# Kernel tuning notes

Measured on AMD Instinct MI355X. Metric: run time of the kernel, lower is better.

The kernel has to match this reference:

```python
import jax, jax.numpy as jnp
import numpy as np

# T time steps, N nodes, R relations, E edges per (t, relation)
T, N, IN_DIM, HID, R, E = 6, 50000, 256, 256, 4, 800000


def setup_inputs() -> dict:
    key = jax.random.key(0)
    ks = jax.random.split(key, 12)
    s = 0.05  # weight scale to keep activations well-conditioned
    return {
        "feat": jax.random.normal(ks[0], (T, N, IN_DIM), jnp.float32),
        "edge_row": jax.random.randint(ks[1], (T, R, E), 0, N, jnp.int32),
        "edge_col": jax.random.randint(ks[2], (T, R, E), 0, N, jnp.int32),
        "edge_w": jax.random.uniform(ks[3], (T, R, E), jnp.float32) * 0.1,
        "W_rel": jax.random.normal(ks[4], (R, IN_DIM, HID), jnp.float32) * s,
        "b_rel": jnp.zeros((R, HID), jnp.float32),
        "rel_query": jax.random.normal(ks[5], (HID,), jnp.float32),
        "gru_W_ih": jax.random.normal(ks[6], (3 * HID, HID), jnp.float32) * s,
        "gru_W_hh": jax.random.normal(ks[7], (3 * HID, HID), jnp.float32) * s,
        "gru_b_ih": jnp.zeros((3 * HID,), jnp.float32),
        "gru_b_hh": jnp.zeros((3 * HID,), jnp.float32),
        "W1": jax.random.normal(ks[8], (HID, HID), jnp.float32) * s,
        "b1": jnp.zeros((HID,), jnp.float32),
        "W2": jax.random.normal(ks[9], (HID, 1), jnp.float32) * s,
        "b2": jnp.zeros((1,), jnp.float32),
    }


def reference(feat, edge_row, edge_col, edge_w, W_rel, b_rel, rel_query,
              gru_W_ih, gru_W_hh, gru_b_ih, gru_b_hh, W1, b1, W2, b2):
    n_nodes = feat.shape[1]
    hid = rel_query.shape[0]

    def spatial(x, row, col, w):
        # per-relation dense transform: [R, N, H]
        z = jnp.einsum('ni,rio->rno', x, W_rel) + b_rel[:, None, :]

        # sparse.mm(A_r, z_r): m[i] = sum_e w_e * z[col_e] scattered to row_e
        def agg(z_r, row_r, col_r, w_r):
            return jax.ops.segment_sum(w_r[:, None] * z_r[col_r], row_r,
                                       num_segments=n_nodes)

        msgs = jax.vmap(agg)(z, row, col, w)  # [R, N, H]
        # relation attention: softmax over relation axis
        alpha = jax.nn.softmax(jnp.einsum('rnh,h->rn', msgs, rel_query), axis=0)
        return jax.nn.relu(jnp.einsum('rn,rnh->nh', alpha, msgs))  # [N, H]

    def gru_step(h, x):
        # torch GRU gate order: r, z, n
        gi = x @ gru_W_ih.T + gru_b_ih  # [N, 3H]
        gh = h @ gru_W_hh.T + gru_b_hh
        ir, iz, inn = jnp.split(gi, 3, axis=-1)
        hr, hz, hn = jnp.split(gh, 3, axis=-1)
        r = jax.nn.sigmoid(ir + hr)
        zg = jax.nn.sigmoid(iz + hz)
        ng = jnp.tanh(inn + r * hn)
        return (1.0 - zg) * ng + zg * h

    def step(h, xs):
        x_t, row_t, col_t, w_t = xs
        return gru_step(h, spatial(x_t, row_t, col_t, w_t)), None

    h0 = jnp.zeros((n_nodes, hid), feat.dtype)
    h_last, _ = jax.lax.scan(step, h0, (feat, edge_row, edge_col, edge_w))

    # classifier (dropout is identity in eval mode)
    h1 = jax.nn.relu(h_last @ W1 + b1)
    return (h1 @ W2 + b2)[:, 0]  # [N]
```

## Files before the change

### kernel.cpp

```cpp
#include <hip/hip_runtime.h>
#include <hip/hip_bf16.h>
#include <math.h>

#define T_STEPS 6
#define N_NODES 50000
#define IN_DIM  256
#define HID     256
#define R_REL   4
#define E_EDGES 800000
#define G3      768
#define MPAD    50048
#define NTR     24
#define ETOT    19200000
#define NTOT    1200000
#define NCB_R   98
#define NCB_TOT 2352
#define CH_BLOCKS 2400
#define CH_EDGES  8000
#define CH_PER_TR 100
#define BCAP    10240

typedef unsigned short ushort_t;
typedef _Float16 f16x8 __attribute__((ext_vector_type(8)));
typedef float  f32x4  __attribute__((ext_vector_type(4)));

__device__ __forceinline__ ushort_t f2h(float v) {
    _Float16 h = (_Float16)v;
    ushort_t u;
    __builtin_memcpy(&u, &h, 2);
    return u;
}
__device__ __forceinline__ float h2f(ushort_t u) {
    _Float16 h;
    __builtin_memcpy(&h, &u, 2);
    return (float)h;
}

__global__ void prep_bt(const float* __restrict__ src, ushort_t* __restrict__ hi,
                        ushort_t* __restrict__ lo, int K, int Nc, int transposed) {
    int idx = blockIdx.x * blockDim.x + threadIdx.x;
    if (idx >= K * Nc) return;
    int n = idx / K, k = idx % K;
    float v = transposed ? src[(size_t)n * K + k] : src[(size_t)k * Nc + n];
    ushort_t hh = f2h(v);
    ushort_t ll = f2h(v - h2f(hh));
    hi[idx] = hh;
    lo[idx] = ll;
}

__global__ void pack_feat_h(const float* __restrict__ f, ushort_t* __restrict__ ph,
                            int total4) {
    int idx = blockIdx.x * blockDim.x + threadIdx.x;
    if (idx >= total4) return;
    float4 v = ((const float4*)f)[idx];
    ushort4 o;
    o.x = f2h(v.x); o.y = f2h(v.y); o.z = f2h(v.z); o.w = f2h(v.w);
    ((ushort4*)ph)[idx] = o;
}


__global__ __launch_bounds__(256)
void coarse_fill(const int* __restrict__ row, const int* __restrict__ col,
                 const float* __restrict__ w, int* __restrict__ gcur,
                 int2* __restrict__ brec) {
    __shared__ int cnt[NCB_R], ofs[NCB_R];
    int tr = blockIdx.x / CH_PER_TR;
    int base = blockIdx.x * CH_EDGES;
    for (int i = threadIdx.x; i < NCB_R; i += 256) cnt[i] = 0;
    __syncthreads();
    for (int k = threadIdx.x; k < CH_EDGES; k += 256)
        atomicAdd(&cnt[row[base + k] >> 9], 1);
    __syncthreads();
    if (threadIdx.x < NCB_R) {
        int c = cnt[threadIdx.x];
        int bk = tr * NCB_R + threadIdx.x;
        int g = c ? atomicAdd(&gcur[bk], c) : 0;
        ofs[threadIdx.x] = bk * BCAP + g;
        cnt[threadIdx.x] = 0;
    }
    __syncthreads();
    for (int k = threadIdx.x; k < CH_EDGES; k += 256) {
        int rr = row[base + k];
        int kb = rr >> 9;
        int pos = ofs[kb] + atomicAdd(&cnt[kb], 1);
        brec[pos] = make_int2(col[base + k] | ((rr & 511) << 16),
                              __float_as_int(w[base + k]));
    }
}

__global__ __launch_bounds__(256)
void place_rows(const int2* __restrict__ brec, const int* __restrict__ gcur,
                int2* __restrict__ starts2, unsigned* __restrict__ colw) {
    __shared__ int cnt[512], rofs[512];
    __shared__ unsigned buf[BCAP];
    int b = blockIdx.x;
    int tr = b / NCB_R, rb = b % NCB_R;
    int row0 = rb << 9;
    int nrows = min(512, N_NODES - row0);
    int s0 = b * BCAP;
    int nrec = min(gcur[b], BCAP);
    for (int i = threadIdx.x; i < 512; i += 256) cnt[i] = 0;
    __syncthreads();
    for (int e = threadIdx.x; e < nrec; e += 256)
        atomicAdd(&cnt[(brec[s0 + e].x >> 16) & 511], 1);
    __syncthreads();
    if (threadIdx.x == 0) {
        int run = 0;
        for (int i = 0; i < 512; ++i) { rofs[i] = run; run += cnt[i]; }
    }
    __syncthreads();
    for (int i = threadIdx.x; i < nrows; i += 256)
        starts2[tr * N_NODES + row0 + i] =
            make_int2(s0 + rofs[i], s0 + rofs[i] + cnt[i]);
    __syncthreads();
    for (int i = threadIdx.x; i < 512; i += 256) cnt[i] = 0;
    __syncthreads();
    for (int e = threadIdx.x; e < nrec; e += 256) {
        int2 rec = brec[s0 + e];
        int rl = (rec.x >> 16) & 511;
        int pos = rofs[rl] + atomicAdd(&cnt[rl], 1);
        buf[pos] = (unsigned)(rec.x & 0xFFFF) |
                   ((unsigned)f2h(__int_as_float(rec.y)) << 16);
    }
    __syncthreads();
    for (int i = threadIdx.x; i < nrec; i += 256)
        colw[s0 + i] = buf[i];
}

__global__ void csr_agg_t(const ushort_t* __restrict__ xh, const unsigned* __restrict__ colw,
                          const int2* __restrict__ startsT,
                          ushort_t* __restrict__ tmp, float* __restrict__ rowsum) {
    int wid  = (blockIdx.x * blockDim.x + threadIdx.x) >> 6;
    int lane = threadIdx.x & 63;
    int r    = blockIdx.y;
    if (wid >= N_NODES) return;
    int2 se = startsT[r * N_NODES + wid];
    int s0 = se.x, s1 = se.y;
    float4 acc = make_float4(0.f, 0.f, 0.f, 0.f);
    float wsum = 0.f;
    const ushort_t* xb = xh + (lane << 2);
    int e = s0;
    for (; e + 8 <= s1; e += 8) {
        unsigned rr[8];
#pragma unroll
        for (int k = 0; k < 8; ++k) rr[k] = colw[e + k];
        ushort4 xv[8];
#pragma unroll
        for (int k = 0; k < 8; ++k)
            xv[k] = *(const ushort4*)(xb + ((size_t)(rr[k] & 0xFFFF) << 8));
#pragma unroll
        for (int k = 0; k < 8; ++k) {
            float wk = h2f((ushort_t)(rr[k] >> 16));
            acc.x = fmaf(wk, h2f(xv[k].x), acc.x);
            acc.y = fmaf(wk, h2f(xv[k].y), acc.y);
            acc.z = fmaf(wk, h2f(xv[k].z), acc.z);
            acc.w = fmaf(wk, h2f(xv[k].w), acc.w);
            wsum += wk;
        }
    }
    for (; e + 4 <= s1; e += 4) {
        unsigned rr[4];
#pragma unroll
        for (int k = 0; k < 4; ++k) rr[k] = colw[e + k];
        ushort4 xv[4];
#pragma unroll
        for (int k = 0; k < 4; ++k)
            xv[k] = *(const ushort4*)(xb + ((size_t)(rr[k] & 0xFFFF) << 8));
#pragma unroll
        for (int k = 0; k < 4; ++k) {
            float wk = h2f((ushort_t)(rr[k] >> 16));
            acc.x = fmaf(wk, h2f(xv[k].x), acc.x);
            acc.y = fmaf(wk, h2f(xv[k].y), acc.y);
            acc.z = fmaf(wk, h2f(xv[k].z), acc.z);
            acc.w = fmaf(wk, h2f(xv[k].w), acc.w);
            wsum += wk;
        }
    }
    for (; e < s1; ++e) {
        unsigned rec = colw[e];
        float we = h2f((ushort_t)(rec >> 16));
        ushort4 xv = *(const ushort4*)(xb + ((size_t)(rec & 0xFFFF) << 8));
        acc.x = fmaf(we, h2f(xv.x), acc.x);
        acc.y = fmaf(we, h2f(xv.y), acc.y);
        acc.z = fmaf(we, h2f(xv.z), acc.z);
        acc.w = fmaf(we, h2f(xv.w), acc.w);
        wsum += we;
    }
    ushort4 hv;
    hv.x = f2h(acc.x); hv.y = f2h(acc.y); hv.z = f2h(acc.z); hv.w = f2h(acc.w);
    *(ushort4*)(tmp + ((size_t)r * MPAD + wid) * 256 + lane * 4) = hv;
    if (lane == 0) rowsum[r * MPAD + wid] = wsum;
}

__global__ __launch_bounds__(256, 3)
void mfma_gemm(const ushort_t* __restrict__ Af, const ushort_t* __restrict__ Bthi,
               const ushort_t* __restrict__ Btlo, void* __restrict__ Cv,
               int M, int Nc, const float* __restrict__ bias,
               const float* __restrict__ rowscale, int do_relu, int out16,
               size_t aZ, size_t bZ, size_t cZ, int biasZ, int rsZ) {
    int z = blockIdx.z;
    Af   += (size_t)z * aZ;
    Bthi += (size_t)z * bZ;  Btlo += (size_t)z * bZ;
    if (bias)     bias     += (size_t)z * biasZ;
    if (rowscale) rowscale += (size_t)z * rsZ;

    __shared__ __align__(16) char smem[49152];
    const int AOF = 0, BHI = 16384, BLO = 32768;
    int tid = threadIdx.x;
    int m0 = blockIdx.x * 128, n0 = blockIdx.y * 128;
    int lane = tid & 63, wid = tid >> 6;
    int wr = wid >> 1, wc = wid & 1;
    int lr = lane & 15, lk = lane >> 4;
    int xorv = (lr & 7) << 4;

    f32x4 acc[4][4];
#pragma unroll
    for (int i = 0; i < 4; ++i)
#pragma unroll
        for (int j = 0; j < 4; ++j)
            acc[i][j] = (f32x4){0.f, 0.f, 0.f, 0.f};

    for (int kt = 0; kt < 4; ++kt) {
        int k0 = kt * 64;
        __syncthreads();
#pragma unroll
        for (int i = 0; i < 4; ++i) {
            int c = tid + i * 256;
            int row = c >> 3, slot = c & 7;
            int ldsoff = row * 128 + ((slot * 16) ^ ((row & 7) << 4));
            size_t ga = (size_t)(m0 + row) * 256 + k0 + slot * 8;
            size_t gb = (size_t)(n0 + row) * 256 + k0 + slot * 8;
            *(int4*)(smem + AOF + ldsoff) = *(const int4*)(Af + ga);
            *(int4*)(smem + BHI + ldsoff) = *(const int4*)(Bthi + gb);
            *(int4*)(smem + BLO + ldsoff) = *(const int4*)(Btlo + gb);
        }
        __syncthreads();
#pragma unroll
        for (int kk2 = 0; kk2 < 2; ++kk2) {
            int kb = (kk2 * 64 + lk * 16) ^ xorv;
            f16x8 a[4], bh[4], bl[4];
#pragma unroll
            for (int f = 0; f < 4; ++f) {
                int ra = (wr * 64 + f * 16 + lr) * 128 + kb;
                int rb = (wc * 64 + f * 16 + lr) * 128 + kb;
                a[f]  = *(const f16x8*)(smem + AOF + ra);
                bh[f] = *(const f16x8*)(smem + BHI + rb);
                bl[f] = *(const f16x8*)(smem + BLO + rb);
            }
#pragma unroll
            for (int fm = 0; fm < 4; ++fm)
#pragma unroll
                for (int fn = 0; fn < 4; ++fn) {
                    acc[fm][fn] = __builtin_amdgcn_mfma_f32_16x16x32_f16(a[fm], bh[fn], acc[fm][fn], 0, 0, 0);
                    acc[fm][fn] = __builtin_amdgcn_mfma_f32_16x16x32_f16(a[fm], bl[fn], acc[fm][fn], 0, 0, 0);
                }
        }
    }
    float*    C32 = (float*)Cv    + (size_t)blockIdx.z * cZ;
    ushort_t* C16 = (ushort_t*)Cv + (size_t)blockIdx.z * cZ;
#pragma unroll
    for (int fm = 0; fm < 4; ++fm) {
        int grb = m0 + wr * 64 + fm * 16 + lk * 4;
#pragma unroll
        for (int j = 0; j < 4; ++j) {
            int gr = grb + j;
            if (gr >= M) continue;
            float rs = rowscale ? rowscale[gr] : 1.0f;
#pragma unroll
            for (int fn = 0; fn < 4; ++fn) {
                int gc = n0 + wc * 64 + fn * 16 + lr;
                float v = acc[fm][fn][j];
                if (bias) v += rs * bias[gc];
                if (do_relu) v = fmaxf(v, 0.f);
                if (out16) C16[(size_t)gr * Nc + gc] = f2h(v);
                else       C32[(size_t)gr * Nc + gc] = v;
            }
        }
    }
}

__global__ void attn_combine(const ushort_t* __restrict__ msgs,
                             const float* __restrict__ q,
                             ushort_t* __restrict__ s_f, int N) {
    int n = blockIdx.x, j = threadIdx.x;
    size_t NH = (size_t)N * 256;
    size_t base = (size_t)n * 256 + j;
    float m0 = h2f(msgs[0 * NH + base]);
    float m1 = h2f(msgs[1 * NH + base]);
    float m2 = h2f(msgs[2 * NH + base]);
    float m3 = h2f(msgs[3 * NH + base]);
    float qv = q[j];
    float v0 = m0 * qv, v1 = m1 * qv, v2 = m2 * qv, v3 = m3 * qv;
#pragma unroll
    for (int off = 32; off; off >>= 1) {
        v0 += __shfl_xor(v0, off);
        v1 += __shfl_xor(v1, off);
        v2 += __shfl_xor(v2, off);
        v3 += __shfl_xor(v3, off);
    }
    __shared__ float part[4][4];
    __shared__ float alpha[4];
    int wid = j >> 6, lane = j & 63;
    if (lane == 0) {
        part[0][wid] = v0; part[1][wid] = v1; part[2][wid] = v2; part[3][wid] = v3;
    }
    __syncthreads();
    if (j == 0) {
        float d[4];
#pragma unroll
        for (int r = 0; r < 4; ++r) d[r] = part[r][0] + part[r][1] + part[r][2] + part[r][3];
        float mx = fmaxf(fmaxf(d[0], d[1]), fmaxf(d[2], d[3]));
        float e[4], sum = 0.f;
#pragma unroll
        for (int r = 0; r < 4; ++r) { e[r] = expf(d[r] - mx); sum += e[r]; }
#pragma unroll
        for (int r = 0; r < 4; ++r) alpha[r] = e[r] / sum;
    }
    __syncthreads();
    float sv = alpha[0] * m0 + alpha[1] * m1 + alpha[2] * m2 + alpha[3] * m3;
    s_f[base] = f2h(fmaxf(sv, 0.f));
}

__global__ void gru_gate(const ushort_t* __restrict__ gi, const ushort_t* __restrict__ gh,
                         float* __restrict__ h, ushort_t* __restrict__ h_f,
                         int total4) {
    int idx = blockIdx.x * blockDim.x + threadIdx.x;
    if (idx >= total4) return;
    int i = idx >> 6, j = (idx & 63) * 4;
    size_t b = (size_t)i * 768 + j;
    ushort4 ir4 = *(const ushort4*)(gi + b);
    ushort4 iz4 = *(const ushort4*)(gi + b + 256);
    ushort4 in4 = *(const ushort4*)(gi + b + 512);
    ushort4 hr4 = *(const ushort4*)(gh + b);
    ushort4 hz4 = *(const ushort4*)(gh + b + 256);
    ushort4 hn4 = *(const ushort4*)(gh + b + 512);
    size_t o = (size_t)i * 256 + j;
    float4 hv = *(const float4*)(h + o);
    float4 hnew;
    const ushort_t* irp = &ir4.x; const ushort_t* izp = &iz4.x; const ushort_t* inp = &in4.x;
    const ushort_t* hrp = &hr4.x; const ushort_t* hzp = &hz4.x; const ushort_t* hnp = &hn4.x;
    const float* hvp = &hv.x; float* hop = &hnew.x;
    ushort4 hf4;
    ushort_t* hfp = &hf4.x;
#pragma unroll
    for (int k = 0; k < 4; ++k) {
        float r = 1.f / (1.f + expf(-(h2f(irp[k]) + h2f(hrp[k]))));
        float z = 1.f / (1.f + expf(-(h2f(izp[k]) + h2f(hzp[k]))));
        float ng = tanhf(h2f(inp[k]) + r * h2f(hnp[k]));
        float v = (1.f - z) * ng + z * hvp[k];
        hop[k] = v;
        hfp[k] = f2h(v);
    }
    *(float4*)(h + o) = hnew;
    *(ushort4*)(h_f + o) = hf4;
}

__global__ void classifier_out(const float* __restrict__ h1, const float* __restrict__ W2,
                               const float* __restrict__ b2, float* __restrict__ out, int N) {
    int n = blockIdx.x, j = threadIdx.x;
    float v = h1[(size_t)n * 256 + j] * W2[j];
#pragma unroll
    for (int off = 32; off; off >>= 1) v += __shfl_xor(v, off);
    __shared__ float part[4];
    if ((j & 63) == 0) part[j >> 6] = v;
    __syncthreads();
    if (j == 0) out[n] = part[0] + part[1] + part[2] + part[3] + b2[0];
}

extern "C" void kernel_launch(void* const* d_in, const int* in_sizes, int n_in,
                              void* d_out, int out_size, void* d_ws, size_t ws_size,
                              hipStream_t stream) {
    const float* feat  = (const float*)d_in[0];
    const int*   erow  = (const int*)d_in[1];
    const int*   ecol  = (const int*)d_in[2];
    const float* ew    = (const float*)d_in[3];
    const float* W_rel = (const float*)d_in[4];
    const float* b_rel = (const float*)d_in[5];
    const float* rq    = (const float*)d_in[6];
    const float* Wih   = (const float*)d_in[7];
    const float* Whh   = (const float*)d_in[8];
    const float* bih   = (const float*)d_in[9];
    const float* bhh   = (const float*)d_in[10];
    const float* W1    = (const float*)d_in[11];
    const float* b1    = (const float*)d_in[12];
    const float* W2    = (const float*)d_in[13];
    const float* b2    = (const float*)d_in[14];
    float* out = (float*)d_out;

    const int N = N_NODES;
    char* ws = (char*)d_ws;

    size_t off_msgs   = 0;
    size_t off_gh     = 102400000;
    size_t off_colw   = 179200000;
    size_t off_h      = 275537920;
    size_t off_hf     = 326737920;
    size_t off_sf     = 352362496;
    size_t off_tmp    = 377987072;
    size_t off_rowsum = 480485376;
    size_t off_wrelh  = 481286144;
    size_t off_wrell  = 481810432;
    size_t off_wihh   = 482334720;
    size_t off_wihl   = 482727936;
    size_t off_whhh   = 483121152;
    size_t off_whhl   = 483514368;
    size_t off_w1h    = 483907584;
    size_t off_w1l    = 484038656;
    size_t off_gcur   = 484169728;
    size_t off_starts = 484179152;
    size_t off_feath  = 493779152;
    size_t off_brec   = 647379168;

    ushort_t* msgs   = (ushort_t*)(ws + off_msgs);
    ushort_t* gi     = (ushort_t*)(ws + off_msgs);
    float*    h1     = (float*)(ws + off_msgs);
    ushort_t* gh     = (ushort_t*)(ws + off_gh);
    unsigned* colw   = (unsigned*)(ws + off_colw);
    float*    h      = (float*)(ws + off_h);
    ushort_t* h_f    = (ushort_t*)(ws + off_hf);
    ushort_t* s_f    = (ushort_t*)(ws + off_sf);
    ushort_t* tmp    = (ushort_t*)(ws + off_tmp);
    float*    rowsum = (float*)(ws + off_rowsum);
    ushort_t* wrel_h = (ushort_t*)(ws + off_wrelh);
    ushort_t* wrel_l = (ushort_t*)(ws + off_wrell);
    ushort_t* wih_h  = (ushort_t*)(ws + off_wihh);
    ushort_t* wih_l  = (ushort_t*)(ws + off_wihl);
    ushort_t* whh_h  = (ushort_t*)(ws + off_whhh);
    ushort_t* whh_l  = (ushort_t*)(ws + off_whhl);
    ushort_t* w1_h   = (ushort_t*)(ws + off_w1h);
    ushort_t* w1_l   = (ushort_t*)(ws + off_w1l);
    int*      gcur   = (int*)(ws + off_gcur);
    int2*     starts2= (int2*)(ws + off_starts);
    ushort_t* feath  = (ushort_t*)(ws + off_feath);
    int2*     brec   = (int2*)(ws + off_brec);

    for (int r = 0; r < R_REL; ++r)
        prep_bt<<<(65536 + 255) / 256, 256, 0, stream>>>(
            W_rel + (size_t)r * 65536, wrel_h + (size_t)r * 65536,
            wrel_l + (size_t)r * 65536, 256, 256, 0);
    prep_bt<<<(G3 * 256 + 255) / 256, 256, 0, stream>>>(Wih, wih_h, wih_l, 256, G3, 1);
    prep_bt<<<(G3 * 256 + 255) / 256, 256, 0, stream>>>(Whh, whh_h, whh_l, 256, G3, 1);
    prep_bt<<<(65536 + 255) / 256, 256, 0, stream>>>(W1, w1_h, w1_l, 256, 256, 0);
    pack_feat_h<<<(T_STEPS * N * IN_DIM / 4 + 255) / 256, 256, 0, stream>>>(
        feat, feath, T_STEPS * N * IN_DIM / 4);

    hipMemsetAsync(h, 0, (size_t)N * HID * 4, stream);
    hipMemsetAsync(ws + off_hf, 0, 25624576, stream);
    hipMemsetAsync(gcur, 0, NCB_TOT * 4, stream);

    coarse_fill<<<CH_BLOCKS, 256, 0, stream>>>(erow, ecol, ew, gcur, brec);
    place_rows<<<NCB_TOT, 256, 0, stream>>>(brec, gcur, starts2, colw);

    dim3 g_rel(MPAD / 128, 2, 4);
    dim3 g_g3(MPAD / 128, 6, 1);
    dim3 g_cls(MPAD / 128, 2, 1);
    dim3 agg_grid((N + 3) / 4, 4);

    for (int t = 0; t < T_STEPS; ++t) {
        const ushort_t* xh_t = feath + (size_t)t * N * IN_DIM;
        csr_agg_t<<<agg_grid, 256, 0, stream>>>(
            xh_t, colw, starts2 + (size_t)t * R_REL * N, tmp, rowsum);
        mfma_gemm<<<g_rel, 256, 0, stream>>>(
            tmp, wrel_h, wrel_l, msgs, N, 256, b_rel, rowsum, 0, 1,
            (size_t)MPAD * 256, 65536, (size_t)N * 256, 256, MPAD);
        attn_combine<<<N, 256, 0, stream>>>(msgs, rq, s_f, N);
        mfma_gemm<<<g_g3, 256, 0, stream>>>(s_f, wih_h, wih_l, gi, N, G3,
                                            bih, nullptr, 0, 1, 0, 0, 0, 0, 0);
        mfma_gemm<<<g_g3, 256, 0, stream>>>(h_f, whh_h, whh_l, gh, N, G3,
                                            bhh, nullptr, 0, 1, 0, 0, 0, 0, 0);
        gru_gate<<<(N * 64 + 255) / 256, 256, 0, stream>>>(gi, gh, h, h_f, N * 64);
    }

    mfma_gemm<<<g_cls, 256, 0, stream>>>(h_f, w1_h, w1_l, h1, N, 256,
                                         b1, nullptr, 1, 0, 0, 0, 0, 0, 0);
    classifier_out<<<N, 256, 0, stream>>>(h1, W2, b2, out, N);
}
```

Baseline: 4.454 ms.

## Pre-pack GEMM weights in MFMA fragment order and load B directly from global

Weight matrices are now repacked into MFMA lane-fragment order (hi/lo fp16 split) so each lane can load its B operand as one 16-byte vector straight from global memory. The GEMM no longer stages B hi/lo through LDS, which cuts shared memory from 48KB to 16KB and removes two thirds of the tile-load traffic into LDS. The cost is that B fragments are re-read from global/L2 per wave on every k step instead of being shared through LDS, and the loads now sit in the inner loop rather than being overlapped with the LDS fill.

```diff
diff --git a/kernel.cpp b/kernel.cpp
--- a/kernel.cpp
+++ b/kernel.cpp
@@ -36,16 +36,17 @@
     return (float)h;
 }
 
-__global__ void prep_bt(const float* __restrict__ src, ushort_t* __restrict__ hi,
-                        ushort_t* __restrict__ lo, int K, int Nc, int transposed) {
-    int idx = blockIdx.x * blockDim.x + threadIdx.x;
-    if (idx >= K * Nc) return;
-    int n = idx / K, k = idx % K;
-    float v = transposed ? src[(size_t)n * K + k] : src[(size_t)k * Nc + n];
+__global__ void prep_bt_pack(const float* __restrict__ src, ushort_t* __restrict__ hi,
+                             ushort_t* __restrict__ lo, int Nc, int transposed) {
+    int p = blockIdx.x * blockDim.x + threadIdx.x;
+    if (p >= Nc * 256) return;
+    int j = p & 7, lane = (p >> 3) & 63, k32 = (p >> 9) & 7, nc16 = p >> 12;
+    int col = nc16 * 16 + (lane & 15);
+    int k   = k32 * 32 + (lane >> 4) * 8 + j;
+    float v = transposed ? src[(size_t)col * 256 + k] : src[(size_t)k * Nc + col];
     ushort_t hh = f2h(v);
-    ushort_t ll = f2h(v - h2f(hh));
-    hi[idx] = hh;
-    lo[idx] = ll;
+    hi[p] = hh;
+    lo[p] = f2h(v - h2f(hh));
 }
 
 __global__ void pack_feat_h(const float* __restrict__ f, ushort_t* __restrict__ ph,
@@ -193,25 +194,25 @@
 }
 
 __global__ __launch_bounds__(256, 3)
-void mfma_gemm(const ushort_t* __restrict__ Af, const ushort_t* __restrict__ Bthi,
-               const ushort_t* __restrict__ Btlo, void* __restrict__ Cv,
+void mfma_gemm(const ushort_t* __restrict__ Af, const ushort_t* __restrict__ Bphi,
+               const ushort_t* __restrict__ Bplo, void* __restrict__ Cv,
                int M, int Nc, const float* __restrict__ bias,
                const float* __restrict__ rowscale, int do_relu, int out16,
                size_t aZ, size_t bZ, size_t cZ, int biasZ, int rsZ) {
     int z = blockIdx.z;
     Af   += (size_t)z * aZ;
-    Bthi += (size_t)z * bZ;  Btlo += (size_t)z * bZ;
+    Bphi += (size_t)z * bZ;  Bplo += (size_t)z * bZ;
     if (bias)     bias     += (size_t)z * biasZ;
     if (rowscale) rowscale += (size_t)z * rsZ;
 
-    __shared__ __align__(16) char smem[49152];
-    const int AOF = 0, BHI = 16384, BLO = 32768;
+    __shared__ __align__(16) char smem[16384];
     int tid = threadIdx.x;
     int m0 = blockIdx.x * 128, n0 = blockIdx.y * 128;
     int lane = tid & 63, wid = tid >> 6;
     int wr = wid >> 1, wc = wid & 1;
     int lr = lane & 15, lk = lane >> 4;
     int xorv = (lr & 7) << 4;
+    int n016 = blockIdx.y * 8;
 
     f32x4 acc[4][4];
 #pragma unroll
@@ -229,23 +230,21 @@
             int row = c >> 3, slot = c & 7;
             int ldsoff = row * 128 + ((slot * 16) ^ ((row & 7) << 4));
             size_t ga = (size_t)(m0 + row) * 256 + k0 + slot * 8;
-            size_t gb = (size_t)(n0 + row) * 256 + k0 + slot * 8;
-            *(int4*)(smem + AOF + ldsoff) = *(const int4*)(Af + ga);
-            *(int4*)(smem + BHI + ldsoff) = *(const int4*)(Bthi + gb);
-            *(int4*)(smem + BLO + ldsoff) = *(const int4*)(Btlo + gb);
+            *(int4*)(smem + ldsoff) = *(const int4*)(Af + ga);
         }
         __syncthreads();
 #pragma unroll
         for (int kk2 = 0; kk2 < 2; ++kk2) {
             int kb = (kk2 * 64 + lk * 16) ^ xorv;
+            int k32 = kt * 2 + kk2;
             f16x8 a[4], bh[4], bl[4];
 #pragma unroll
             for (int f = 0; f < 4; ++f) {
                 int ra = (wr * 64 + f * 16 + lr) * 128 + kb;
-                int rb = (wc * 64 + f * 16 + lr) * 128 + kb;
-                a[f]  = *(const f16x8*)(smem + AOF + ra);
-                bh[f] = *(const f16x8*)(smem + BHI + rb);
-                bl[f] = *(const f16x8*)(smem + BLO + rb);
+                a[f]  = *(const f16x8*)(smem + ra);
+                size_t bo = ((size_t)((n016 + wc * 4 + f) * 8 + k32) * 64 + lane) * 8;
+                bh[f] = *(const f16x8*)(Bphi + bo);
+                bl[f] = *(const f16x8*)(Bplo + bo);
             }
 #pragma unroll
             for (int fm = 0; fm < 4; ++fm)
@@ -435,12 +434,12 @@
     int2*     brec   = (int2*)(ws + off_brec);
 
     for (int r = 0; r < R_REL; ++r)
-        prep_bt<<<(65536 + 255) / 256, 256, 0, stream>>>(
+        prep_bt_pack<<<(65536 + 255) / 256, 256, 0, stream>>>(
             W_rel + (size_t)r * 65536, wrel_h + (size_t)r * 65536,
-            wrel_l + (size_t)r * 65536, 256, 256, 0);
-    prep_bt<<<(G3 * 256 + 255) / 256, 256, 0, stream>>>(Wih, wih_h, wih_l, 256, G3, 1);
-    prep_bt<<<(G3 * 256 + 255) / 256, 256, 0, stream>>>(Whh, whh_h, whh_l, 256, G3, 1);
-    prep_bt<<<(65536 + 255) / 256, 256, 0, stream>>>(W1, w1_h, w1_l, 256, 256, 0);
+            wrel_l + (size_t)r * 65536, 256, 0);
+    prep_bt_pack<<<(G3 * 256 + 255) / 256, 256, 0, stream>>>(Wih, wih_h, wih_l, G3, 1);
+    prep_bt_pack<<<(G3 * 256 + 255) / 256, 256, 0, stream>>>(Whh, whh_h, whh_l, G3, 1);
+    prep_bt_pack<<<(65536 + 255) / 256, 256, 0, stream>>>(W1, w1_h, w1_l, 256, 0);
     pack_feat_h<<<(T_STEPS * N * IN_DIM / 4 + 255) / 256, 256, 0, stream>>>(
         feat, feath, T_STEPS * N * IN_DIM / 4);
 
```

After: 4.570 ms. +2.6%, slower.
